# Kernel tuning notes

Hardware: AMD Instinct MI355X
Metric: run time of the kernel (lower is better)

Reference implementation:

```python
import jax, jax.numpy as jnp
import numpy as np

# Mamba2 hyperparameters
D_MODEL = 768
D_STATE = 64
D_CONV = 4
EXPAND = 2
HEADDIM = 64
CHUNK = 64
D_INNER = EXPAND * D_MODEL            # 1536
NHEADS = D_INNER // HEADDIM           # 24
D_IN_PROJ = 2 * D_INNER + 2 * D_STATE + NHEADS  # 3224
CONV_DIM = D_INNER + 2 * D_STATE      # 1664
B_SZ = 8
SEQ = 4096  # multiple of CHUNK -> no padding branch


def setup_inputs() -> dict:
    key = jax.random.key(0)
    ks = jax.random.split(key, 6)
    u = jax.random.normal(ks[0], (B_SZ, SEQ, D_MODEL), jnp.float32)
    # fan-in scaled weights (matches nn.Linear/Conv1d default init scale)
    W_in = jax.random.normal(ks[1], (D_IN_PROJ, D_MODEL), jnp.float32) / np.sqrt(D_MODEL).astype(np.float32)
    conv_w = jax.random.normal(ks[2], (CONV_DIM, 1, D_CONV), jnp.float32) / np.sqrt(D_CONV).astype(np.float32)
    conv_b = jnp.zeros((CONV_DIM,), jnp.float32)
    dt_bias = jax.random.uniform(ks[3], (NHEADS,), jnp.float32, -4.0, 1.0)  # nn.init.uniform_(-4, 1)
    A_log = jnp.full((NHEADS,), -np.log(2.0), jnp.float32)                  # nn.init.constant_(-log 2)
    D_param = jnp.ones((NHEADS,), jnp.float32)
    norm_w = jnp.ones((D_INNER,), jnp.float32)
    W_out = jax.random.normal(ks[4], (D_MODEL, D_INNER), jnp.float32) / np.sqrt(D_INNER).astype(np.float32)
    return dict(u=u, W_in=W_in, conv_w=conv_w, conv_b=conv_b, dt_bias=dt_bias,
                A_log=A_log, D_param=D_param, norm_w=norm_w, W_out=W_out)


def _segsum(x):
    """Stable segment sum: out[..., i, j] = sum_{j < k <= i} x[..., k]; -inf above diagonal."""
    T = x.shape[-1]
    lower_strict = jnp.tril(jnp.ones((T, T), bool), -1)
    xe = jnp.where(lower_strict, x[..., :, None], 0.0)   # broadcast x over last (col) axis
    s = jnp.cumsum(xe, axis=-2)
    lower = jnp.tril(jnp.ones((T, T), bool), 0)
    return jnp.where(lower, s, -jnp.inf)


def _ssd(x, A, B, C, chunk):
    """Chunked SSD. x:(b,L,h,p)  A:(b,L,h)  B,C:(b,L,1,n)."""
    b, L, h, p = x.shape
    c = L // chunk
    n = B.shape[-1]
    x = x.reshape(b, c, chunk, h, p)
    A = A.reshape(b, c, chunk, h).transpose(0, 3, 1, 2)   # b h c l
    B = B.reshape(b, c, chunk, 1, n)
    C = C.reshape(b, c, chunk, 1, n)
    A_cs = jnp.cumsum(A, axis=-1)                          # b h c l
    # intra-chunk (diagonal) term
    Lmat = jnp.exp(_segsum(A))                             # b h c l s
    Y_diag = jnp.einsum('bclhn,bcshn,bhcls,bcshp->bclhp', C, B, Lmat, x)
    # per-chunk states
    decay_states = jnp.exp(A_cs[..., -1:] - A_cs)          # b h c l
    states = jnp.einsum('bclhn,bhcl,bclhp->bchpn', B, decay_states, x)
    states = jnp.concatenate([jnp.zeros_like(states[:, :1]), states], axis=1)  # b (c+1) h p n
    # inter-chunk recurrence
    A_last = jnp.pad(A_cs[..., -1], ((0, 0), (0, 0), (1, 0)))  # b h (c+1)
    decay_chunk = jnp.exp(_segsum(A_last))                     # b h (c+1) (c+1)
    new_states = jnp.einsum('bhzc,bchpn->bzhpn', decay_chunk, states)
    states = new_states[:, :-1]                                # b c h p n
    # off-diagonal (state-to-output) term
    Y_off = jnp.einsum('bclhn,bchpn,bhcl->bclhp', C, states, jnp.exp(A_cs))
    return (Y_diag + Y_off).reshape(b, L, h, p)


def reference(u, W_in, conv_w, conv_b, dt_bias, A_log, D_param, norm_w, W_out):
    b, L, _ = u.shape  # L % CHUNK == 0, so pad branch is a no-op
    zxbcdt = u @ W_in.T                                    # (b, L, D_IN_PROJ)
    z = zxbcdt[..., :D_INNER]
    xBC = zxbcdt[..., D_INNER:D_INNER + CONV_DIM]
    dt = jax.nn.softplus(zxbcdt[..., D_INNER + CONV_DIM:] + dt_bias)  # (b, L, h)
    # causal depthwise conv1d (torch pads both sides by d_conv-1 then slices [:L] == left pad)
    xBC = jax.lax.conv_general_dilated(
        xBC.transpose(0, 2, 1), conv_w, window_strides=(1,),
        padding=[(D_CONV - 1, 0)], dimension_numbers=('NCH', 'OIH', 'NCH'),
        feature_group_count=CONV_DIM)
    xBC = jax.nn.silu(xBC.transpose(0, 2, 1) + conv_b)     # (b, L, CONV_DIM)
    x = xBC[..., :D_INNER].reshape(b, L, NHEADS, HEADDIM)
    Bm = xBC[..., D_INNER:D_INNER + D_STATE][:, :, None, :]  # (b, L, 1, n)
    Cm = xBC[..., D_INNER + D_STATE:][:, :, None, :]
    A = -jnp.exp(A_log)                                    # (h,)
    Y = _ssd(x * dt[..., None], A * dt, Bm, Cm, CHUNK)
    y = Y + x * D_param[:, None]                           # skip term
    y = y.reshape(b, L, D_INNER)
    # gated RMSNorm: x * silu(z), then rmsnorm * weight
    y = y * jax.nn.silu(z)
    y = y * jax.lax.rsqrt(jnp.mean(y * y, axis=-1, keepdims=True) + 1e-5) * norm_w
    return y @ W_out.T
```

## Files before the change

kernel.cpp:

```cpp
#include <hip/hip_runtime.h>
#include <stdint.h>

typedef unsigned short u16;
typedef __bf16 bf16x8 __attribute__((ext_vector_type(8)));
typedef float f32x4 __attribute__((ext_vector_type(4)));
typedef unsigned short u16x8 __attribute__((ext_vector_type(8)));
typedef unsigned short u16x4 __attribute__((ext_vector_type(4)));
typedef __attribute__((address_space(1))) unsigned int gu32;
typedef __attribute__((address_space(3))) unsigned int lu32;

__device__ __forceinline__ float bf2f(u16 u){ unsigned int v=((unsigned int)u)<<16; float f; __builtin_memcpy(&f,&v,4); return f; }
__device__ __forceinline__ u16 f2bf(float f){ unsigned int v; __builtin_memcpy(&v,&f,4); v += 0x7fffu + ((v>>16)&1u); return (u16)(v>>16); }
__device__ __forceinline__ int swz(int r,int c){ return (r<<6) + (c ^ ((r&7)<<3)); }
__device__ __forceinline__ void glds16(const void* g, void* l){
  __builtin_amdgcn_global_load_lds((gu32*)g, (lu32*)l, 16, 0, 0);
}

__global__ __launch_bounds__(256) void k_cast(const float* __restrict__ in, u16* __restrict__ out, int n4){
  int i = blockIdx.x*256 + threadIdx.x;
  if (i >= n4) return;
  const f32x4 v = *(const f32x4*)(in + (size_t)i*4);
  u16x4 o; o.x=f2bf(v.x); o.y=f2bf(v.y); o.z=f2bf(v.z); o.w=f2bf(v.w);
  *(u16x4*)(out + (size_t)i*4) = o;
}

__global__ __launch_bounds__(256) void k_cast_pad(const float* __restrict__ in, u16* __restrict__ out){
  int i = blockIdx.x*256 + threadIdx.x;
  int e0 = i*4;
  int row = e0 / 768;
  int col = e0 - row*768;
  u16x4 o;
  if (row < 3224){
    const f32x4 v = *(const f32x4*)(in + (size_t)row*768 + col);
    o.x=f2bf(v.x); o.y=f2bf(v.y); o.z=f2bf(v.z); o.w=f2bf(v.w);
  } else { o.x=0; o.y=0; o.z=0; o.w=0; }
  *(u16x4*)(out + e0) = o;
}

template<int K, int EPI>
__global__ __launch_bounds__(256,2) void k_gemm(
    const u16* __restrict__ A, const u16* __restrict__ Bw,
    u16* __restrict__ o_z, u16* __restrict__ o_xbc, float* __restrict__ o_dt,
    const float* __restrict__ dt_bias, float* __restrict__ o_f32)
{
  __shared__ __align__(16) u16 Alds[8192];
  __shared__ __align__(16) u16 Blds[8192];
  const int tid = threadIdx.x;
  const int wave = tid>>6, lane = tid&63;
  const int m0 = blockIdx.x<<7, n0 = blockIdx.y<<7;
  const int wr = (wave>>1)<<6, wc = (wave&1)<<6;
  const int srow = tid>>3, sc0 = (tid&7)<<3;
  const int lo16 = lane&15, hi = lane>>4;
  f32x4 acc[4][4] = {};
  for (int k0 = 0; k0 < K; k0 += 64){
    #pragma unroll
    for (int i = 0; i < 4; ++i){
      const int row = (i<<5) + srow;
      const int scol = sc0 ^ ((row&7)<<3);
      glds16(A  + (size_t)(m0+row)*K + k0 + scol, &Alds[(i<<11) + (wave<<9)]);
      glds16(Bw + (size_t)(n0+row)*K + k0 + scol, &Blds[(i<<11) + (wave<<9)]);
    }
    __syncthreads();
    #pragma unroll
    for (int kk = 0; kk < 2; ++kk){
      const int kb = (kk<<5) + (hi<<3);
      bf16x8 af[4], bfv[4];
      #pragma unroll
      for (int m = 0; m < 4; ++m){
        const int r = wr + (m<<4) + lo16;
        af[m] = *(const bf16x8*)&Alds[(r<<6) + (kb ^ ((r&7)<<3))];
      }
      #pragma unroll
      for (int n = 0; n < 4; ++n){
        const int r = wc + (n<<4) + lo16;
        bfv[n] = *(const bf16x8*)&Blds[(r<<6) + (kb ^ ((r&7)<<3))];
      }
      #pragma unroll
      for (int m = 0; m < 4; ++m)
      #pragma unroll
      for (int n = 0; n < 4; ++n)
        acc[m][n] = __builtin_amdgcn_mfma_f32_16x16x32_bf16(af[m], bfv[n], acc[m][n], 0,0,0);
    }
    __syncthreads();
  }
  #pragma unroll
  for (int m = 0; m < 4; ++m)
  #pragma unroll
  for (int n = 0; n < 4; ++n)
  #pragma unroll
  for (int i = 0; i < 4; ++i){
    const int gr = m0 + wr + (m<<4) + (hi<<2) + i;
    const int gc = n0 + wc + (n<<4) + lo16;
    const float v = acc[m][n][i];
    if constexpr (EPI == 0){
      if (gc < 1536)      o_z[(size_t)gr*1536 + gc] = f2bf(v);
      else if (gc < 3200) o_xbc[(size_t)gr*1664 + (gc-1536)] = f2bf(v);
      else if (gc < 3224){
        const float t = v + dt_bias[gc-3200];
        o_dt[(size_t)(gc-3200)*32768 + gr] = (t > 20.f) ? t : log1pf(__expf(t));
      }
    } else {
      o_f32[(size_t)gr*768 + gc] = v;
    }
  }
}

__global__ __launch_bounds__(256) void k_conv(
    const u16* __restrict__ xbc, const float* __restrict__ cw, const float* __restrict__ cb,
    const float* __restrict__ dtT,
    u16* __restrict__ xT, u16* __restrict__ Bn, u16* __restrict__ BT, u16* __restrict__ Cn)
{
  const int idx = blockIdx.x*256 + threadIdx.x;
  if (idx >= 4096*208) return;
  const int g  = idx % 208;
  const int pt = idx / 208;
  const int ch0 = g << 3;
  const int m0 = pt << 3;
  const int l0 = m0 & 4095;
  float wgt[8][4], bias8[8];
  #pragma unroll
  for (int j = 0; j < 8; ++j){
    const f32x4 wv = *(const f32x4*)(cw + (size_t)(ch0+j)*4);
    wgt[j][0]=wv.x; wgt[j][1]=wv.y; wgt[j][2]=wv.z; wgt[j][3]=wv.w;
    bias8[j] = cb[ch0+j];
  }
  float acc[8][8];
  #pragma unroll
  for (int p = 0; p < 8; ++p)
  #pragma unroll
  for (int j = 0; j < 8; ++j) acc[p][j] = bias8[j];
  #pragma unroll
  for (int r = -3; r < 8; ++r){
    const int ls = l0 + r;
    if (ls < 0) continue;
    const u16x8 v = *(const u16x8*)(xbc + (size_t)(m0+r)*1664 + ch0);
    float xf[8];
    #pragma unroll
    for (int j = 0; j < 8; ++j) xf[j] = bf2f(v[j]);
    #pragma unroll
    for (int t = 0; t < 4; ++t){
      const int p = r + 3 - t;
      if (p < 0 || p > 7) continue;
      #pragma unroll
      for (int j = 0; j < 8; ++j) acc[p][j] += xf[j] * wgt[j][t];
    }
  }
  #pragma unroll
  for (int p = 0; p < 8; ++p)
  #pragma unroll
  for (int j = 0; j < 8; ++j){ const float s = acc[p][j]; acc[p][j] = s / (1.f + __expf(-s)); }

  const int b = m0 >> 12;
  const int cch = l0 >> 6;
  const int lr0 = l0 & 63;
  if (ch0 < 1536){
    const int h = ch0 >> 6, p0 = ch0 & 63;
    const f32x4 d0 = *(const f32x4*)(dtT + (size_t)h*32768 + m0);
    const f32x4 d1 = *(const f32x4*)(dtT + (size_t)h*32768 + m0 + 4);
    const float dtl[8] = {d0.x,d0.y,d0.z,d0.w,d1.x,d1.y,d1.z,d1.w};
    const size_t rb = (size_t)(b*24+h)*64;
    #pragma unroll
    for (int j = 0; j < 8; ++j){
      const int row = p0 + j;
      u16x8 o;
      #pragma unroll
      for (int p = 0; p < 8; ++p) o[p] = f2bf(acc[p][j] * dtl[p]);
      *(u16x8*)(xT + (rb + row)*4096 + (size_t)cch*64 + (lr0 ^ ((row&7)<<3))) = o;
    }
  } else if (ch0 < 1600){
    const int n0 = ch0 - 1536;
    const size_t tb = ((size_t)(b*64 + cch))*4096;
    #pragma unroll
    for (int p = 0; p < 8; ++p){
      const int lr = lr0 + p;
      u16x8 o;
      #pragma unroll
      for (int j = 0; j < 8; ++j) o[j] = f2bf(acc[p][j]);
      *(u16x8*)(Bn + tb + lr*64 + (n0 ^ ((lr&7)<<3))) = o;
    }
    #pragma unroll
    for (int j = 0; j < 8; ++j){
      const int row = n0 + j;
      u16x8 o;
      #pragma unroll
      for (int p = 0; p < 8; ++p) o[p] = f2bf(acc[p][j]);
      *(u16x8*)(BT + tb + row*64 + (lr0 ^ ((row&7)<<3))) = o;
    }
  } else {
    const int n0 = ch0 - 1600;
    const size_t tb = ((size_t)(b*64 + cch))*4096;
    #pragma unroll
    for (int p = 0; p < 8; ++p){
      const int lr = lr0 + p;
      u16x8 o;
      #pragma unroll
      for (int j = 0; j < 8; ++j) o[j] = f2bf(acc[p][j]);
      *(u16x8*)(Cn + tb + lr*64 + (n0 ^ ((lr&7)<<3))) = o;
    }
  }
}

__global__ __launch_bounds__(256,1) void k_ssd(
    const u16* __restrict__ xT, const u16* __restrict__ Bn, const u16* __restrict__ BT,
    const u16* __restrict__ Cn, const float* __restrict__ dtT, const float* __restrict__ A_log,
    const float* __restrict__ Dp, u16* __restrict__ yo)
{
  __shared__ __align__(16) u16 tiles[2][4][4096];
  __shared__ __align__(16) u16 Ml[4096];
  __shared__ __align__(16) u16 Sbf[4096];
  __shared__ float Sst[4096];
  __shared__ float df[64], Acs[64], decs[64], els[64];
  const int tid = threadIdx.x, wave = tid>>6, lane = tid&63;
  const int lo16 = lane&15, hi = lane>>4;
  const int b = blockIdx.x / 24, h = blockIdx.x % 24;
  const float Ah = -__expf(A_log[h]);
  const float Dh = Dp[h];
  for (int i = tid; i < 4096; i += 256){ Sst[i]=0.f; Sbf[i]=0; }
  const size_t xTg  = (size_t)(b*24+h)*64*4096;
  const size_t bcg  = (size_t)b*64*4096;
  const size_t dtg0 = (size_t)h*32768 + (size_t)b*4096;
  const size_t yb   = (size_t)b*4096*1536 + (size_t)h*64;

  auto stage = [&](int buf, int c){
    u16* dst = &tiles[buf][wave][0];
    if (wave == 0){
      const u16* g0 = xT + xTg + (size_t)c*64 + (size_t)(lane>>3)*4096 + (lane&7)*8;
      #pragma unroll
      for (int s = 0; s < 8; ++s) glds16(g0 + (size_t)s*32768, dst + s*512);
    } else {
      const u16* src = (wave==1 ? Bn : wave==2 ? BT : Cn) + bcg + (size_t)c*4096 + lane*8;
      #pragma unroll
      for (int s = 0; s < 8; ++s) glds16(src + s*512, dst + s*512);
    }
  };

  float dtc = dtT[dtg0 + lane];
  stage(0, 0);

  for (int c = 0; c < 64; ++c){
    float s = Ah * dtc;
    #pragma unroll
    for (int o = 1; o < 64; o <<= 1){ const float t = __shfl_up(s, o); if (lane >= o) s += t; }
    const float Alast = __shfl(s, 63);
    const float lam = __expf(Alast);
    if (wave == 0){ df[lane] = dtc; Acs[lane] = s; decs[lane] = __expf(Alast - s); els[lane] = __expf(s); }
    if (c < 63){
      dtc = dtT[dtg0 + (size_t)(c+1)*64 + lane];
      stage((c+1)&1, c+1);
    }
    if (c == 0)       asm volatile("s_waitcnt vmcnt(0) lgkmcnt(0)" ::: "memory");
    else if (c == 63) asm volatile("s_waitcnt vmcnt(16) lgkmcnt(0)" ::: "memory");
    else              asm volatile("s_waitcnt vmcnt(25) lgkmcnt(0)" ::: "memory");
    __builtin_amdgcn_s_barrier();

    const u16* tx = &tiles[c&1][0][0];
    const u16* tb = &tiles[c&1][1][0];
    const u16* tt = &tiles[c&1][2][0];
    const u16* tc = &tiles[c&1][3][0];

    f32x4 accG[4] = {};
    #pragma unroll
    for (int kk = 0; kk < 2; ++kk){
      const int kb = (kk<<5) + (hi<<3);
      const int rA = (wave<<4) + lo16;
      const bf16x8 a = *(const bf16x8*)&tc[(rA<<6) + (kb ^ ((rA&7)<<3))];
      #pragma unroll
      for (int t = 0; t < 4; ++t){
        const int rb = (t<<4) + lo16;
        const bf16x8 bb = *(const bf16x8*)&tb[(rb<<6) + (kb ^ ((rb&7)<<3))];
        accG[t] = __builtin_amdgcn_mfma_f32_16x16x32_bf16(a, bb, accG[t], 0,0,0);
      }
    }
    #pragma unroll
    for (int t = 0; t < 4; ++t)
    #pragma unroll
    for (int i = 0; i < 4; ++i){
      const int r = (wave<<4) + (hi<<2) + i;
      const int sc = (t<<4) + lo16;
      float v = 0.f;
      if (sc <= r) v = accG[t][i] * __expf(Acs[r] - Acs[sc]);
      if (sc == r) v += Dh / df[r];
      Ml[swz(r,sc)] = f2bf(v);
    }
    f32x4 aYd[4] = {}, aYo[4] = {}, aS[4] = {};
    #pragma unroll
    for (int kk = 0; kk < 2; ++kk){
      const int kb = (kk<<5) + (hi<<3);
      const int rA = (wave<<4) + lo16;
      const int oA = (rA<<6) + (kb ^ ((rA&7)<<3));
      const bf16x8 aM = *(const bf16x8*)&Ml[oA];
      const bf16x8 aC = *(const bf16x8*)&tc[oA];
      const u16x8  aXu = *(const u16x8*)&tx[oA];
      u16x8 aXsu;
      #pragma unroll
      for (int j = 0; j < 8; ++j) aXsu[j] = f2bf(bf2f(aXu[j]) * decs[kb + j]);
      const bf16x8 aXs = *(const bf16x8*)&aXsu;
      #pragma unroll
      for (int t = 0; t < 4; ++t){
        const int rb = (t<<4) + lo16;
        const int o = (rb<<6) + (kb ^ ((rb&7)<<3));
        const bf16x8 bX = *(const bf16x8*)&tx[o];
        const bf16x8 bS = *(const bf16x8*)&Sbf[o];
        const bf16x8 bB = *(const bf16x8*)&tt[o];
        aYd[t] = __builtin_amdgcn_mfma_f32_16x16x32_bf16(aM, bX, aYd[t], 0,0,0);
        aYo[t] = __builtin_amdgcn_mfma_f32_16x16x32_bf16(aC, bS, aYo[t], 0,0,0);
        aS[t]  = __builtin_amdgcn_mfma_f32_16x16x32_bf16(aXs, bB, aS[t], 0,0,0);
      }
    }
    float el4[4];
    #pragma unroll
    for (int i = 0; i < 4; ++i) el4[i] = els[(wave<<4) + (hi<<2) + i];
    asm volatile("s_waitcnt lgkmcnt(0)" ::: "memory");
    __builtin_amdgcn_s_barrier();
    #pragma unroll
    for (int t = 0; t < 4; ++t)
    #pragma unroll
    for (int i = 0; i < 4; ++i){
      const int p = (wave<<4) + (hi<<2) + i;
      const int n = (t<<4) + lo16;
      const float sv = Sst[(p<<6)+n] * lam + aS[t][i];
      Sst[(p<<6)+n] = sv;
      Sbf[swz(p,n)] = f2bf(sv);
    }
    #pragma unroll
    for (int t = 0; t < 4; ++t)
    #pragma unroll
    for (int i = 0; i < 4; ++i){
      const int r = (wave<<4) + (hi<<2) + i;
      const int p = (t<<4) + lo16;
      const float y = aYd[t][i] + el4[i] * aYo[t][i];
      yo[yb + (size_t)((c<<6)+r)*1536 + p] = f2bf(y);
    }
  }
}

__global__ __launch_bounds__(192) void k_gnorm(
    const u16* __restrict__ y, const u16* __restrict__ z,
    const float* __restrict__ nw, u16* __restrict__ out)
{
  __shared__ float red[3];
  const int m = blockIdx.x, t = threadIdx.x;
  const size_t base = (size_t)m*1536 + t*8;
  const u16x8 yv = *(const u16x8*)(y + base);
  const u16x8 zv = *(const u16x8*)(z + base);
  float vals[8]; float ss = 0.f;
  #pragma unroll
  for (int j = 0; j < 8; ++j){
    const float zf = bf2f(zv[j]);
    const float v = bf2f(yv[j]) * zf / (1.f + __expf(-zf));
    vals[j] = v; ss += v*v;
  }
  #pragma unroll
  for (int off = 32; off > 0; off >>= 1) ss += __shfl_down(ss, off);
  if ((t & 63) == 0) red[t>>6] = ss;
  __syncthreads();
  const float sc = rsqrtf((red[0]+red[1]+red[2]) * (1.f/1536.f) + 1e-5f);
  u16x8 o;
  #pragma unroll
  for (int j = 0; j < 8; ++j) o[j] = f2bf(vals[j] * sc * nw[t*8+j]);
  *(u16x8*)(out + base) = o;
}

extern "C" void kernel_launch(void* const* d_in, const int* in_sizes, int n_in,
                              void* d_out, int out_size, void* d_ws, size_t ws_size,
                              hipStream_t stream)
{
  const float* u       = (const float*)d_in[0];
  const float* W_in    = (const float*)d_in[1];
  const float* conv_w  = (const float*)d_in[2];
  const float* conv_b  = (const float*)d_in[3];
  const float* dt_bias = (const float*)d_in[4];
  const float* A_log   = (const float*)d_in[5];
  const float* D_param = (const float*)d_in[6];
  const float* norm_w  = (const float*)d_in[7];
  const float* W_out   = (const float*)d_in[8];
  (void)in_sizes; (void)n_in; (void)out_size;
  if (ws_size < (size_t)379715584) return;

  char* w = (char*)d_ws;
  size_t off = 0;
  auto alloc = [&](size_t bytes)->void*{ void* p = w + off; off += (bytes + 255) & ~(size_t)255; return p; };
  u16* ubf    = (u16*)alloc(50331648);
  u16* winbf  = (u16*)alloc(5111808);
  u16* woutbf = (u16*)alloc(2359296);
  u16* zbf    = (u16*)alloc(100663296);
  u16* xbcbf  = (u16*)alloc(109051904);
  float* dtT  = (float*)alloc(3145728);
  u16* xTb    = (u16*)alloc(100663296);
  u16* Bnb    = (u16*)alloc(4194304);
  u16* Cnb    = (u16*)alloc(4194304);
  u16* BTb    = ubf;
  u16* yssd   = xbcbf;
  u16* ynorm  = xTb;

  k_cast<<<24576, 256, 0, stream>>>(u, ubf, 6291456);
  k_cast_pad<<<2496, 256, 0, stream>>>(W_in, winbf);
  k_cast<<<1152, 256, 0, stream>>>(W_out, woutbf, 294912);
  k_gemm<768,0><<<dim3(256,26), 256, 0, stream>>>(ubf, winbf, zbf, xbcbf, dtT, dt_bias, nullptr);
  k_conv<<<3328, 256, 0, stream>>>(xbcbf, conv_w, conv_b, dtT, xTb, Bnb, BTb, Cnb);
  k_ssd<<<192, 256, 0, stream>>>(xTb, Bnb, BTb, Cnb, dtT, A_log, D_param, yssd);
  k_gnorm<<<32768, 192, 0, stream>>>(yssd, zbf, norm_w, ynorm);
  k_gemm<1536,1><<<dim3(256,6), 256, 0, stream>>>(ynorm, woutbf, nullptr, nullptr, nullptr, nullptr, (float*)d_out);
}
```

Baseline: 773.4 us.

## Transpose SSD MFMA roles, keep state in registers, vectorize stores, relax waits

Reworks the per-chunk SSD kernel so the MFMA operand roles are swapped, and the outputs come out transposed (columns per lane). This allows packed u16x4 stores to Ml, Sbf and the y output, and reuses the C fragments across two matmuls. The fp32 running state moves from shared memory into registers, and the per-chunk scalars (cumsum, decay, dt) are broadcast with shuffles instead of going through shared arrays. The vmcnt wait thresholds are also loosened, and an extra barrier is added after the Ml write. The cost is higher register pressure, and the tight vmcnt counts are fragile and could cause races if the load counts differ from what is assumed.

```diff
diff --git a/kernel.cpp b/kernel.cpp
--- a/kernel.cpp
+++ b/kernel.cpp
@@ -208,14 +208,14 @@
   __shared__ __align__(16) u16 tiles[2][4][4096];
   __shared__ __align__(16) u16 Ml[4096];
   __shared__ __align__(16) u16 Sbf[4096];
-  __shared__ float Sst[4096];
-  __shared__ float df[64], Acs[64], decs[64], els[64];
   const int tid = threadIdx.x, wave = tid>>6, lane = tid&63;
   const int lo16 = lane&15, hi = lane>>4;
+  const int w16 = wave<<4, hi4 = hi<<2;
   const int b = blockIdx.x / 24, h = blockIdx.x % 24;
   const float Ah = -__expf(A_log[h]);
   const float Dh = Dp[h];
-  for (int i = tid; i < 4096; i += 256){ Sst[i]=0.f; Sbf[i]=0; }
+  for (int i = tid; i < 4096; i += 256) Sbf[i] = 0;
+  f32x4 Sreg[4] = {};
   const size_t xTg  = (size_t)(b*24+h)*64*4096;
   const size_t bcg  = (size_t)b*64*4096;
   const size_t dtg0 = (size_t)h*32768 + (size_t)b*4096;
@@ -242,15 +242,17 @@
     #pragma unroll
     for (int o = 1; o < 64; o <<= 1){ const float t = __shfl_up(s, o); if (lane >= o) s += t; }
     const float Alast = __shfl(s, 63);
-    const float lam = __expf(Alast);
-    if (wave == 0){ df[lane] = dtc; Acs[lane] = s; decs[lane] = __expf(Alast - s); els[lane] = __expf(s); }
+    const float lam  = __expf(Alast);
+    const float decl = __expf(Alast - s);
+    const float elv  = __expf(s);
+    float dtn = 0.f;
     if (c < 63){
-      dtc = dtT[dtg0 + (size_t)(c+1)*64 + lane];
+      dtn = dtT[dtg0 + (size_t)(c+1)*64 + lane];
       stage((c+1)&1, c+1);
     }
-    if (c == 0)       asm volatile("s_waitcnt vmcnt(0) lgkmcnt(0)" ::: "memory");
-    else if (c == 63) asm volatile("s_waitcnt vmcnt(16) lgkmcnt(0)" ::: "memory");
-    else              asm volatile("s_waitcnt vmcnt(25) lgkmcnt(0)" ::: "memory");
+    if (c == 0)       asm volatile("s_waitcnt vmcnt(9)  lgkmcnt(0)" ::: "memory");
+    else if (c == 63) asm volatile("s_waitcnt vmcnt(4)  lgkmcnt(0)" ::: "memory");
+    else              asm volatile("s_waitcnt vmcnt(13) lgkmcnt(0)" ::: "memory");
     __builtin_amdgcn_s_barrier();
 
     const u16* tx = &tiles[c&1][0][0];
@@ -259,78 +261,92 @@
     const u16* tc = &tiles[c&1][3][0];
 
     f32x4 accG[4] = {};
+    bf16x8 bfC[2][4];
     #pragma unroll
     for (int kk = 0; kk < 2; ++kk){
       const int kb = (kk<<5) + (hi<<3);
-      const int rA = (wave<<4) + lo16;
-      const bf16x8 a = *(const bf16x8*)&tc[(rA<<6) + (kb ^ ((rA&7)<<3))];
+      const int rA = w16 + lo16;
+      const bf16x8 aB = *(const bf16x8*)&tb[(rA<<6) + (kb ^ ((rA&7)<<3))];
       #pragma unroll
       for (int t = 0; t < 4; ++t){
         const int rb = (t<<4) + lo16;
-        const bf16x8 bb = *(const bf16x8*)&tb[(rb<<6) + (kb ^ ((rb&7)<<3))];
-        accG[t] = __builtin_amdgcn_mfma_f32_16x16x32_bf16(a, bb, accG[t], 0,0,0);
-      }
-    }
-    #pragma unroll
-    for (int t = 0; t < 4; ++t)
-    #pragma unroll
-    for (int i = 0; i < 4; ++i){
-      const int r = (wave<<4) + (hi<<2) + i;
-      const int sc = (t<<4) + lo16;
-      float v = 0.f;
-      if (sc <= r) v = accG[t][i] * __expf(Acs[r] - Acs[sc]);
-      if (sc == r) v += Dh / df[r];
-      Ml[swz(r,sc)] = f2bf(v);
-    }
+        bfC[kk][t] = *(const bf16x8*)&tc[(rb<<6) + (kb ^ ((rb&7)<<3))];
+        accG[t] = __builtin_amdgcn_mfma_f32_16x16x32_bf16(aB, bfC[kk][t], accG[t], 0,0,0);
+      }
+    }
+    float As_i[4];
+    #pragma unroll
+    for (int i = 0; i < 4; ++i) As_i[i] = __shfl(s, w16 + hi4 + i);
+    #pragma unroll
+    for (int t = 0; t < 4; ++t){
+      const int l = (t<<4) + lo16;
+      const float Al  = __shfl(s, l);
+      const float dtl = __shfl(dtc, l);
+      u16x4 ov;
+      #pragma unroll
+      for (int i = 0; i < 4; ++i){
+        const int si = w16 + hi4 + i;
+        float v = 0.f;
+        if (si <= l) v = accG[t][i] * __expf(Al - As_i[i]);
+        if (si == l) v += Dh / dtl;
+        ov[i] = f2bf(v);
+      }
+      *(u16x4*)&Ml[(l<<6) + ((w16 + hi4) ^ ((l&7)<<3))] = ov;
+    }
+    asm volatile("s_waitcnt lgkmcnt(0)" ::: "memory");
+    __builtin_amdgcn_s_barrier();
+
     f32x4 aYd[4] = {}, aYo[4] = {}, aS[4] = {};
     #pragma unroll
     for (int kk = 0; kk < 2; ++kk){
       const int kb = (kk<<5) + (hi<<3);
-      const int rA = (wave<<4) + lo16;
+      const int rA = w16 + lo16;
       const int oA = (rA<<6) + (kb ^ ((rA&7)<<3));
-      const bf16x8 aM = *(const bf16x8*)&Ml[oA];
-      const bf16x8 aC = *(const bf16x8*)&tc[oA];
-      const u16x8  aXu = *(const u16x8*)&tx[oA];
-      u16x8 aXsu;
-      #pragma unroll
-      for (int j = 0; j < 8; ++j) aXsu[j] = f2bf(bf2f(aXu[j]) * decs[kb + j]);
-      const bf16x8 aXs = *(const bf16x8*)&aXsu;
+      const bf16x8 aX = *(const bf16x8*)&tx[oA];
+      const bf16x8 aSb= *(const bf16x8*)&Sbf[oA];
+      const u16x8 aBTu= *(const u16x8*)&tt[oA];
+      u16x8 aBTs;
+      #pragma unroll
+      for (int j = 0; j < 8; ++j) aBTs[j] = f2bf(bf2f(aBTu[j]) * __shfl(decl, kb + j));
+      const bf16x8 aBT = *(const bf16x8*)&aBTs;
       #pragma unroll
       for (int t = 0; t < 4; ++t){
         const int rb = (t<<4) + lo16;
         const int o = (rb<<6) + (kb ^ ((rb&7)<<3));
+        const bf16x8 bM = *(const bf16x8*)&Ml[o];
         const bf16x8 bX = *(const bf16x8*)&tx[o];
-        const bf16x8 bS = *(const bf16x8*)&Sbf[o];
-        const bf16x8 bB = *(const bf16x8*)&tt[o];
-        aYd[t] = __builtin_amdgcn_mfma_f32_16x16x32_bf16(aM, bX, aYd[t], 0,0,0);
-        aYo[t] = __builtin_amdgcn_mfma_f32_16x16x32_bf16(aC, bS, aYo[t], 0,0,0);
-        aS[t]  = __builtin_amdgcn_mfma_f32_16x16x32_bf16(aXs, bB, aS[t], 0,0,0);
-      }
-    }
-    float el4[4];
-    #pragma unroll
-    for (int i = 0; i < 4; ++i) el4[i] = els[(wave<<4) + (hi<<2) + i];
+        aYd[t] = __builtin_amdgcn_mfma_f32_16x16x32_bf16(aX,  bM,         aYd[t], 0,0,0);
+        aYo[t] = __builtin_amdgcn_mfma_f32_16x16x32_bf16(aSb, bfC[kk][t], aYo[t], 0,0,0);
+        aS[t]  = __builtin_amdgcn_mfma_f32_16x16x32_bf16(aBT, bX,         aS[t],  0,0,0);
+      }
+    }
     asm volatile("s_waitcnt lgkmcnt(0)" ::: "memory");
     __builtin_amdgcn_s_barrier();
-    #pragma unroll
-    for (int t = 0; t < 4; ++t)
-    #pragma unroll
-    for (int i = 0; i < 4; ++i){
-      const int p = (wave<<4) + (hi<<2) + i;
-      const int n = (t<<4) + lo16;
-      const float sv = Sst[(p<<6)+n] * lam + aS[t][i];
-      Sst[(p<<6)+n] = sv;
-      Sbf[swz(p,n)] = f2bf(sv);
-    }
-    #pragma unroll
-    for (int t = 0; t < 4; ++t)
-    #pragma unroll
-    for (int i = 0; i < 4; ++i){
-      const int r = (wave<<4) + (hi<<2) + i;
+
+    #pragma unroll
+    for (int t = 0; t < 4; ++t){
       const int p = (t<<4) + lo16;
-      const float y = aYd[t][i] + el4[i] * aYo[t][i];
-      yo[yb + (size_t)((c<<6)+r)*1536 + p] = f2bf(y);
-    }
+      u16x4 sv;
+      #pragma unroll
+      for (int i = 0; i < 4; ++i){
+        const float nv = Sreg[t][i] * lam + aS[t][i];
+        Sreg[t][i] = nv;
+        sv[i] = f2bf(nv);
+      }
+      *(u16x4*)&Sbf[(p<<6) + ((w16 + hi4) ^ ((p&7)<<3))] = sv;
+    }
+    #pragma unroll
+    for (int t = 0; t < 4; ++t){
+      const int l = (t<<4) + lo16;
+      const float el = elv;
+      (void)el;
+      const float elt = __shfl(elv, l);
+      u16x4 ov;
+      #pragma unroll
+      for (int i = 0; i < 4; ++i) ov[i] = f2bf(aYd[t][i] + elt * aYo[t][i]);
+      *(u16x4*)(yo + yb + (size_t)((c<<6)+l)*1536 + w16 + hi4) = ov;
+    }
+    dtc = dtn;
   }
 }
 
```

New measurement: 738.1 us. -4.6%, faster.
